# Optimization experiments

Hardware: AMD Instinct MI355X
Metric: run time of the kernel (lower is better)

Reference implementation:

```python
import jax, jax.numpy as jnp
import numpy as np

C = 768
NH = 8
S_SP = 9            # spatial size per axis; seq = 9**3 = 729
HID = (C * 4 * 2) // 3  # 2048, floor(768*8/3)
E = 3               # num_experts
TOPK = 2
EPS = 1e-5


def setup_inputs() -> dict:
    key = jax.random.key(0)
    ks = jax.random.split(key, 10)
    b = 8
    p = lambda k, shape: (jax.random.normal(k, shape, dtype=jnp.float32) * 0.02)
    return {
        "x": jax.random.normal(ks[0], (b, C, S_SP, S_SP, S_SP), dtype=jnp.float32),
        "ln_w": jnp.ones((C, S_SP, S_SP, S_SP), dtype=jnp.float32),
        "ln_b": jnp.zeros((C, S_SP, S_SP, S_SP), dtype=jnp.float32),
        "qkv_w": p(ks[1], (C, 3 * C)),
        "proj_w": p(ks[2], (C, C)),
        "router_w": p(ks[3], (C, E)),
        "gate_w": p(ks[4], (E, C, HID)),
        "up_w": p(ks[5], (E, C, HID)),
        "down_w": p(ks[6], (E, HID, C)),
    }


def _ablock(x, ln_w, ln_b, qkv_w, proj_w, router_w, gate_w, up_w, down_w):
    b, c, t, h, w = x.shape
    s = t * h * w
    dh = c // NH

    # LayerNorm over normalized_shape = (c, t, h, w)
    mean = jnp.mean(x, axis=(1, 2, 3, 4), keepdims=True)
    var = jnp.var(x, axis=(1, 2, 3, 4), keepdims=True)
    y = (x - mean) * jax.lax.rsqrt(var + EPS) * ln_w + ln_b

    # Attention (note: source applies NO 1/sqrt(dh) scaling)
    tok = jnp.transpose(y.reshape(b, c, s), (0, 2, 1))        # (b, s, c)
    qkv = (tok @ qkv_w).reshape(b, s, 3, NH, dh)
    qkv = jnp.transpose(qkv, (2, 0, 3, 1, 4))                  # (3, b, nh, s, dh)
    q, k, v = qkv[0], qkv[1], qkv[2]
    attn = jax.nn.softmax(jnp.einsum("bhsd,bhtd->bhst", q, k), axis=-1)
    o = jnp.einsum("bhst,bhtd->bhsd", attn, v)
    o = jnp.transpose(o, (0, 2, 1, 3)).reshape(b, s, c) @ proj_w  # (b, s, c)
    x = x + jnp.transpose(o, (0, 2, 1)).reshape(b, c, t, h, w)

    # MoE with top-2 routing over SwiGLU experts (dense compute)
    tok = jnp.transpose(x.reshape(b, c, s), (0, 2, 1))         # (b, s, c)
    probs = jax.nn.softmax(tok @ router_w, axis=-1)            # (b, s, E)
    vals, idx = jax.lax.top_k(probs, TOPK)
    vals = vals / jnp.sum(vals, axis=-1, keepdims=True)
    wfull = jnp.sum(jax.nn.one_hot(idx, E, dtype=tok.dtype) * vals[..., None], axis=2)  # (b, s, E)

    g = jnp.einsum("bsc,ech->bseh", tok, gate_w)
    u = jnp.einsum("bsc,ech->bseh", tok, up_w)
    hid = jax.nn.silu(g) * u                                   # (b, s, E, HID)
    eo = jnp.einsum("bseh,ehc->bsec", hid, down_w)             # (b, s, E, c)
    moe_out = jnp.einsum("bsec,bse->bsc", eo, wfull)

    return x + jnp.transpose(moe_out, (0, 2, 1)).reshape(b, c, t, h, w)


def reference(x, ln_w, ln_b, qkv_w, proj_w, router_w, gate_w, up_w, down_w):
    return _ablock(x, ln_w, ln_b, qkv_w, proj_w, router_w, gate_w, up_w, down_w)
```

## Files before the change

kernel.cpp:

```cpp
#include <hip/hip_runtime.h>
#include <hip/hip_bf16.h>

#define C_    768
#define NH_   8
#define DH_   96
#define S_    729
#define B_    8
#define MTOK  5832
#define C3    2304
#define GUN   12288
#define DK    6144
#define SPAD  736
#define NPB   559872

typedef __attribute__((ext_vector_type(8))) short short8;
typedef __attribute__((ext_vector_type(4))) float f32x4;
typedef __attribute__((ext_vector_type(4))) unsigned int uint4v;
typedef __hip_bfloat16 bf16;

__device__ __forceinline__ void gld_lds16(const bf16* g, bf16* l) {
  __builtin_amdgcn_global_load_lds((const __attribute__((address_space(1))) void*)g,
                                   (__attribute__((address_space(3))) void*)l, 16, 0, 0);
}
__device__ __forceinline__ void gld_lds16c(const char* g, char* l) {
  __builtin_amdgcn_global_load_lds((const __attribute__((address_space(1))) void*)g,
                                   (__attribute__((address_space(3))) void*)l, 16, 0, 0);
}

template<int DBO>
__device__ __forceinline__ void g97_step(
    char* ldsc, char* ldsw, const int rA, const int rB, const int cx,
    const char*& pA0, const char*& pA1, const char*& pB0, const char*& pB1,
    const bool stage, f32x4 (&acc)[4][4])
{
  const int NBO = 16384 - DBO;
  if (stage) {
    gld_lds16c(pA0, ldsw + NBO);
    gld_lds16c(pA1, ldsw + NBO + 4096);
    gld_lds16c(pB0, ldsw + NBO + 8192);
    gld_lds16c(pB1, ldsw + NBO + 12288);
    pA0 += 64; pA1 += 64; pB0 += 64; pB1 += 64;
  }
  short8 a4[4], b4[4];
  #pragma unroll
  for (int mf = 0; mf < 4; ++mf)
    a4[mf] = *(const short8*)(ldsc + DBO + rA + mf*1024 + cx);
  #pragma unroll
  for (int nf = 0; nf < 4; ++nf)
    b4[nf] = *(const short8*)(ldsc + DBO + rB + nf*1024 + cx);
  __builtin_amdgcn_s_setprio(1);
  #pragma unroll
  for (int mf = 0; mf < 4; ++mf)
    #pragma unroll
    for (int nf = 0; nf < 4; ++nf)
      acc[mf][nf] = __builtin_amdgcn_mfma_f32_16x16x32_bf16(a4[mf], b4[nf], acc[mf][nf], 0, 0, 0);
  __builtin_amdgcn_s_setprio(0);
  asm volatile("s_waitcnt vmcnt(0)" ::: "memory");
  __builtin_amdgcn_s_barrier();
}

__global__ void __launch_bounds__(256, 4)
gemm97(const bf16* __restrict__ A, long a_rs,
       const bf16* __restrict__ Bt, long b_rs,
       float* __restrict__ Cf, bf16* __restrict__ Cb,
       long c_rs, long c_zoff, int M, int N, int Ksub,
       const float* __restrict__ wfull, int mode)
{
  __shared__ __attribute__((aligned(128))) char ldsc[32768];
  const int tid = threadIdx.x;
  const int wid = tid >> 6, lid = tid & 63;
  const int wm = wid >> 1, wn = wid & 1;
  const int fr = lid & 15, g8 = (lid >> 4) * 8;
  const int brow = blockIdx.y * 128, bcol = blockIdx.x * 128;
  const long k0b = (long)blockIdx.z * Ksub * 2;
  const long a_rsb = a_rs * 2, b_rsb = b_rs * 2;
  const int srow = tid >> 2;
  const int scol = ((tid & 3) ^ ((tid >> 3) & 3)) << 4;
  const int NT = Ksub >> 5;
  char* ldsw = ldsc + wid * 1024;

  int ra0_ = brow + srow;       if (ra0_ > M-1) ra0_ = M-1;
  int ra1_ = brow + 64 + srow;  if (ra1_ > M-1) ra1_ = M-1;
  int rb0_ = bcol + srow;       if (rb0_ > N-1) rb0_ = N-1;
  int rb1_ = bcol + 64 + srow;  if (rb1_ > N-1) rb1_ = N-1;
  const char* pA0 = (const char*)A + (long)ra0_*a_rsb + k0b + scol;
  const char* pA1 = (const char*)A + (long)ra1_*a_rsb + k0b + scol;
  const char* pB0 = (const char*)Bt + (long)rb0_*b_rsb + k0b + scol;
  const char* pB1 = (const char*)Bt + (long)rb1_*b_rsb + k0b + scol;

  const int cx = (g8*2) ^ (((fr >> 1) & 3) << 4);
  const int rA = (wm*64 + fr)*64;
  const int rB = 8192 + (wn*64 + fr)*64;

  f32x4 acc[4][4] = {};

  gld_lds16c(pA0, ldsw);
  gld_lds16c(pA1, ldsw + 4096);
  gld_lds16c(pB0, ldsw + 8192);
  gld_lds16c(pB1, ldsw + 12288);
  pA0 += 64; pA1 += 64; pB0 += 64; pB1 += 64;
  asm volatile("s_waitcnt vmcnt(0)" ::: "memory");
  __builtin_amdgcn_s_barrier();

  for (int tp = 0; tp < NT; tp += 2) {
    g97_step<0>(ldsc, ldsw, rA, rB, cx, pA0, pA1, pB0, pB1, true, acc);
    g97_step<16384>(ldsc, ldsw, rA, rB, cx, pA0, pA1, pB0, pB1, (tp + 2) < NT, acc);
  }

  const int rg = (lid >> 4) * 4;
  if (mode == 3) {
    #pragma unroll
    for (int mf = 0; mf < 4; ++mf) {
      #pragma unroll
      for (int np = 0; np < 2; ++np) {
        const int hb = (bcol + wn*64 + np*32) >> 5;
        const int h = hb*16 + fr;
        const int e = h >> 11;
        #pragma unroll
        for (int j = 0; j < 4; ++j) {
          const int row = brow + wm*64 + mf*16 + rg + j;
          if (row < M) {
            float g = acc[mf][2*np][j];
            float u = acc[mf][2*np+1][j];
            float w = wfull[row*3 + e];
            float sg = g / (1.f + __expf(-g));
            Cb[(long)row*c_rs + h] = __float2bfloat16(sg * u * w);
          }
        }
      }
    }
  } else {
    #pragma unroll
    for (int mf = 0; mf < 4; ++mf) {
      #pragma unroll
      for (int nf = 0; nf < 4; ++nf) {
        const int col = bcol + wn*64 + nf*16 + fr;
        if (col < N) {
          #pragma unroll
          for (int j = 0; j < 4; ++j) {
            const int row = brow + wm*64 + mf*16 + rg + j;
            if (row < M) {
              long off = (long)blockIdx.z*c_zoff + (long)row*c_rs + col;
              if (mode == 0) Cb[off] = __float2bfloat16(acc[mf][nf][j]);
              else           Cf[off] = acc[mf][nf][j];
            }
          }
        }
      }
    }
  }
}

__global__ void __launch_bounds__(256, 3)
gemm3_bt(const bf16* __restrict__ Ah, const bf16* __restrict__ Al,
         long a_rs, long a_oo, long a_oi,
         const bf16* __restrict__ Bth, const bf16* __restrict__ Btl,
         long b_rs, long b_oo, long b_oi,
         float* __restrict__ Cf, bf16* __restrict__ Ch, bf16* __restrict__ Cl,
         long c_rs, long c_oo, long c_oi,
         int M, int N, int K, int nlim, int zdiv)
{
  __shared__ bf16 lAh[4096];
  __shared__ bf16 lAl[4096];
  __shared__ bf16 lBh[4096];
  __shared__ bf16 lBl[4096];
  const int tid = threadIdx.x;
  const int wid = tid >> 6;
  const int lid = tid & 63;
  const int z = blockIdx.z;
  const int zo = z / zdiv, zi = z - zo*zdiv;
  const long aoff = (long)zo*a_oo + (long)zi*a_oi;
  const long boff = (long)zo*b_oo + (long)zi*b_oi;
  const long cbase = (long)zo*c_oo + (long)zi*c_oi;
  const int brow = blockIdx.y * 128;
  const int bcol = blockIdx.x * 128;

  const int ch0 = tid, ch1 = tid + 256;
  int ra0 = brow + (ch0 >> 2); if (ra0 > M-1) ra0 = M-1;
  int ra1 = brow + (ch1 >> 2); if (ra1 > M-1) ra1 = M-1;
  int rb0 = bcol + (ch0 >> 2); if (rb0 > N-1) rb0 = N-1;
  int rb1 = bcol + (ch1 >> 2); if (rb1 > N-1) rb1 = N-1;
  const int sw = ((ch0 ^ (ch0 >> 3)) & 3) * 8;
  const char* qh0 = (const char*)(Ah + aoff + (long)ra0*a_rs + sw);
  const char* qh1 = (const char*)(Ah + aoff + (long)ra1*a_rs + sw);
  const char* ql0 = (const char*)(Al + aoff + (long)ra0*a_rs + sw);
  const char* ql1 = (const char*)(Al + aoff + (long)ra1*a_rs + sw);
  const char* rh0 = (const char*)(Bth + boff + (long)rb0*b_rs + sw);
  const char* rh1 = (const char*)(Bth + boff + (long)rb1*b_rs + sw);
  const char* rl0 = (const char*)(Btl + boff + (long)rb0*b_rs + sw);
  const char* rl1 = (const char*)(Btl + boff + (long)rb1*b_rs + sw);
  char* dAh0 = (char*)lAh + wid*1024;
  char* dAh1 = (char*)lAh + 4096 + wid*1024;
  char* dAl0 = (char*)lAl + wid*1024;
  char* dAl1 = (char*)lAl + 4096 + wid*1024;
  char* dBh0 = (char*)lBh + wid*1024;
  char* dBh1 = (char*)lBh + 4096 + wid*1024;
  char* dBl0 = (char*)lBl + wid*1024;
  char* dBl1 = (char*)lBl + 4096 + wid*1024;

  f32x4 acc[4][4] = {};
  const int wm = wid >> 1, wn = wid & 1;
  const int fr = lid & 15, g8 = (lid >> 4) * 8;
  const int gx = g8 ^ (((lid >> 1) & 3) << 3);

  const int NTk = K >> 5;
  for (int kt = 0; kt < NTk; ++kt) {
    __syncthreads();
    gld_lds16c(qh0, dAh0);
    gld_lds16c(qh1, dAh1);
    gld_lds16c(ql0, dAl0);
    gld_lds16c(ql1, dAl1);
    gld_lds16c(rh0, dBh0);
    gld_lds16c(rh1, dBh1);
    gld_lds16c(rl0, dBl0);
    gld_lds16c(rl1, dBl1);
    qh0 += 64; qh1 += 64; ql0 += 64; ql1 += 64;
    rh0 += 64; rh1 += 64; rl0 += 64; rl1 += 64;
    __syncthreads();
    short8 fah[4], fal[4], fbh[4], fbl[4];
    #pragma unroll
    for (int m = 0; m < 4; ++m) {
      int ro = (wm*64 + m*16 + fr)*32 + gx;
      fah[m] = *(const short8*)&lAh[ro];
      fal[m] = *(const short8*)&lAl[ro];
    }
    #pragma unroll
    for (int n = 0; n < 4; ++n) {
      int ro = (wn*64 + n*16 + fr)*32 + gx;
      fbh[n] = *(const short8*)&lBh[ro];
      fbl[n] = *(const short8*)&lBl[ro];
    }
    #pragma unroll
    for (int m = 0; m < 4; ++m)
      #pragma unroll
      for (int n = 0; n < 4; ++n) {
        acc[m][n] = __builtin_amdgcn_mfma_f32_16x16x32_bf16(fal[m], fbh[n], acc[m][n], 0, 0, 0);
        acc[m][n] = __builtin_amdgcn_mfma_f32_16x16x32_bf16(fah[m], fbl[n], acc[m][n], 0, 0, 0);
        acc[m][n] = __builtin_amdgcn_mfma_f32_16x16x32_bf16(fah[m], fbh[n], acc[m][n], 0, 0, 0);
      }
  }

  const int rg = (lid >> 4) * 4;
  #pragma unroll
  for (int m = 0; m < 4; ++m) {
    #pragma unroll
    for (int n = 0; n < 4; ++n) {
      const int col = bcol + wn*64 + n*16 + fr;
      if (col < nlim) {
        #pragma unroll
        for (int j = 0; j < 4; ++j) {
          const int row = brow + wm*64 + m*16 + rg + j;
          if (row < M) {
            long off = cbase + (long)row*c_rs + col;
            float v = acc[m][n][j];
            if (Cl) {
              bf16 h = __float2bfloat16(v);
              Ch[off] = h;
              Cl[off] = __float2bfloat16(v - __bfloat162float(h));
            } else if (Ch) {
              Ch[off] = __float2bfloat16(v);
            } else {
              Cf[off] = v;
            }
          }
        }
      }
    }
  }
}

__global__ void wtrans(const float* __restrict__ in, bf16* __restrict__ out,
                       int R, int Cc, long in_rs, long out_rs, long in_bs, long out_bs,
                       int ilv, int radd)
{
  __shared__ float tile[32][33];
  in  += (long)blockIdx.z * in_bs;
  out += (long)blockIdx.z * out_bs;
  int r0 = blockIdx.y*32, c0 = blockIdx.x*32;
  int tx = threadIdx.x, ty = threadIdx.y;
  #pragma unroll
  for (int i = 0; i < 32; i += 8) {
    int r = r0 + ty + i, c = c0 + tx;
    if (r < R && c < Cc) tile[ty+i][tx] = in[(long)r*in_rs + c];
  }
  __syncthreads();
  #pragma unroll
  for (int i = 0; i < 32; i += 8) {
    int ro = c0 + ty + i, co = r0 + tx;
    if (ro < Cc && co < R) {
      int rr = ilv ? (((ro >> 4) << 5) + (ro & 15) + radd) : ro;
      out[(long)rr*out_rs + co] = __float2bfloat16(tile[tx][ty+i]);
    }
  }
}

__global__ void wtrans3(const float* __restrict__ in, bf16* __restrict__ oh, bf16* __restrict__ ol,
                        int R, int Cc, long in_rs, long out_rs)
{
  __shared__ float tile[32][33];
  int r0 = blockIdx.y*32, c0 = blockIdx.x*32;
  int tx = threadIdx.x, ty = threadIdx.y;
  #pragma unroll
  for (int i = 0; i < 32; i += 8) {
    int r = r0 + ty + i, c = c0 + tx;
    if (r < R && c < Cc) tile[ty+i][tx] = in[(long)r*in_rs + c];
  }
  __syncthreads();
  #pragma unroll
  for (int i = 0; i < 32; i += 8) {
    int ro = c0 + ty + i, co = r0 + tx;
    if (ro < Cc && co < R) {
      float v = tile[tx][ty+i];
      bf16 h = __float2bfloat16(v);
      long o = (long)ro*out_rs + co;
      oh[o] = h;
      ol[o] = __float2bfloat16(v - __bfloat162float(h));
    }
  }
}

__global__ void ln_partial(const float* __restrict__ x, float* __restrict__ part) {
  int b = blockIdx.y, blk = blockIdx.x;
  const float* xb = x + (long)b*NPB;
  int start = blk * 4374;
  float s = 0.f, ss = 0.f;
  for (int i = start + threadIdx.x; i < start + 4374; i += 256) {
    float v = xb[i]; s += v; ss += v*v;
  }
  #pragma unroll
  for (int o = 32; o; o >>= 1) { s += __shfl_down(s, o); ss += __shfl_down(ss, o); }
  __shared__ float red[2][4];
  int wid = threadIdx.x >> 6, lid = threadIdx.x & 63;
  if (lid == 0) { red[0][wid] = s; red[1][wid] = ss; }
  __syncthreads();
  if (threadIdx.x == 0) {
    float S = 0.f, SS = 0.f;
    for (int w = 0; w < 4; ++w) { S += red[0][w]; SS += red[1][w]; }
    part[(b*128 + blk)*2] = S; part[(b*128 + blk)*2 + 1] = SS;
  }
}

__global__ void ln_final(const float* __restrict__ part, float* __restrict__ stats) {
  int b = blockIdx.x, lid = threadIdx.x;
  float s = 0.f, ss = 0.f;
  for (int i = lid; i < 128; i += 64) { s += part[(b*128+i)*2]; ss += part[(b*128+i)*2+1]; }
  #pragma unroll
  for (int o = 32; o; o >>= 1) { s += __shfl_down(s, o); ss += __shfl_down(ss, o); }
  if (lid == 0) {
    float mean = s / (float)NPB;
    float var = ss / (float)NPB - mean*mean;
    stats[b*2] = mean; stats[b*2+1] = rsqrtf(var + 1e-5f);
  }
}

__global__ void ln_apply3(const float* __restrict__ x, const float* __restrict__ lnw,
                          const float* __restrict__ lnb, const float* __restrict__ stats,
                          bf16* __restrict__ th, bf16* __restrict__ tl, long ts)
{
  __shared__ float tile[32][33];
  int b = blockIdx.z;
  int s0 = blockIdx.x*32, c0 = blockIdx.y*32;
  float mean = stats[b*2], rstd = stats[b*2+1];
  int tx = threadIdx.x, ty = threadIdx.y;
  #pragma unroll
  for (int i = 0; i < 32; i += 8) {
    int c = c0 + ty + i, s = s0 + tx;
    if (s < S_) {
      long o = (long)c*S_ + s;
      tile[ty+i][tx] = (x[(long)b*NPB + o] - mean)*rstd*lnw[o] + lnb[o];
    }
  }
  __syncthreads();
  #pragma unroll
  for (int i = 0; i < 32; i += 8) {
    int s = s0 + ty + i, c = c0 + tx;
    if (s < S_) {
      float v = tile[tx][ty+i];
      bf16 h = __float2bfloat16(v);
      long o = ((long)b*S_ + s)*ts + c;
      th[o] = h;
      tl[o] = __float2bfloat16(v - __bfloat162float(h));
    }
  }
}

__global__ void vtrans2(const bf16* __restrict__ qkvh, const bf16* __restrict__ qkvl,
                        bf16* __restrict__ VTh, bf16* __restrict__ VTl)
{
  __shared__ float tile[32][33];
  int z = blockIdx.z;
  const bf16* qkv = (z < 64) ? qkvh : qkvl;
  bf16* VT = (z < 64) ? VTh : VTl;
  int zz = z & 63;
  int bb = zz >> 3, h = zz & 7;
  const bf16* v = qkv + (long)bb*S_*C3 + 1536 + h*DH_;
  bf16* o = VT + (long)zz*DH_*SPAD;
  int t0 = blockIdx.y*32, d0 = blockIdx.x*32;
  int tx = threadIdx.x, ty = threadIdx.y;
  #pragma unroll
  for (int i = 0; i < 32; i += 8) {
    int t = t0 + ty + i, d = d0 + tx;
    float val = 0.f;
    if (t < S_ && d < DH_) val = __bfloat162float(v[(long)t*C3 + d]);
    tile[ty+i][tx] = val;
  }
  __syncthreads();
  #pragma unroll
  for (int i = 0; i < 32; i += 8) {
    int d = d0 + ty + i, t = t0 + tx;
    if (d < DH_ && t < SPAD) o[(long)d*SPAD + t] = __float2bfloat16(tile[tx][ty+i]);
  }
}

__global__ void softmax3p(bf16* __restrict__ scores, int nrows) {
  int row = blockIdx.x*4 + (threadIdx.x >> 6);
  if (row >= nrows) return;
  int lid = threadIdx.x & 63;
  bf16* ph = scores + (long)row*2*SPAD;
  bf16* pl = ph + SPAD;
  float vals[12];
  float mx = -1e30f;
  #pragma unroll
  for (int i = 0; i < 12; ++i) {
    int t = i*64 + lid;
    float v = -1e30f;
    if (t < S_) v = __bfloat162float(ph[t]) + __bfloat162float(pl[t]);
    vals[i] = v; mx = fmaxf(mx, v);
  }
  #pragma unroll
  for (int o = 32; o; o >>= 1) mx = fmaxf(mx, __shfl_xor(mx, o));
  float sum = 0.f;
  #pragma unroll
  for (int i = 0; i < 12; ++i) { float e = __expf(vals[i] - mx); vals[i] = e; sum += e; }
  #pragma unroll
  for (int o = 32; o; o >>= 1) sum += __shfl_xor(sum, o);
  float inv = 1.f / sum;
  #pragma unroll
  for (int i = 0; i < 12; ++i) {
    int t = i*64 + lid;
    if (t < SPAD) {
      float p = (t < S_) ? vals[i]*inv : 0.f;
      bf16 h = __float2bfloat16(p);
      ph[t] = h;
      pl[t] = __float2bfloat16(p - __bfloat162float(h));
    }
  }
}

__global__ void tadd1(const float* __restrict__ x, const float* __restrict__ oproj,
                      float* __restrict__ xattn, bf16* __restrict__ tok2,
                      float* __restrict__ tok2f)
{
  __shared__ float t_o[32][33];
  __shared__ float t_x[32][33];
  int b = blockIdx.z;
  int s0 = blockIdx.x*32, c0 = blockIdx.y*32;
  int tx = threadIdx.x, ty = threadIdx.y;
  #pragma unroll
  for (int i = 0; i < 32; i += 8) {
    int s = s0 + ty + i;
    if (s < S_) t_o[ty+i][tx] = oproj[((long)b*S_ + s)*C_ + c0 + tx];
    int s2 = s0 + tx;
    if (s2 < S_) t_x[ty+i][tx] = x[(long)b*NPB + (long)(c0+ty+i)*S_ + s2];
  }
  __syncthreads();
  #pragma unroll
  for (int i = 0; i < 32; i += 8) {
    int s = s0 + tx, c = c0 + ty + i;
    if (s < S_) xattn[(long)b*NPB + (long)c*S_ + s] = t_x[ty+i][tx] + t_o[tx][ty+i];
    int s2 = s0 + ty + i, c2 = c0 + tx;
    if (s2 < S_) {
      float v = t_x[tx][ty+i] + t_o[ty+i][tx];
      long o = ((long)b*S_ + s2)*C_ + c2;
      tok2[o] = __float2bfloat16(v);
      tok2f[o] = v;
    }
  }
}

__global__ void tadd2(const float* __restrict__ xattn, const bf16* __restrict__ prt,
                      float* __restrict__ out)
{
  __shared__ float t_m[32][33];
  __shared__ float t_x[32][33];
  int b = blockIdx.z;
  int s0 = blockIdx.x*32, c0 = blockIdx.y*32;
  int tx = threadIdx.x, ty = threadIdx.y;
  #pragma unroll
  for (int i = 0; i < 32; i += 8) {
    int s = s0 + ty + i;
    if (s < S_) {
      const bf16* p = prt + ((long)b*S_ + s)*768 + c0 + tx;
      float acc = 0.f;
      #pragma unroll
      for (int z = 0; z < 8; ++z) acc += __bfloat162float(p[(long)z*MTOK*768]);
      t_m[ty+i][tx] = acc;
    }
    int s2 = s0 + tx;
    if (s2 < S_) t_x[ty+i][tx] = xattn[(long)b*NPB + (long)(c0+ty+i)*S_ + s2];
  }
  __syncthreads();
  #pragma unroll
  for (int i = 0; i < 32; i += 8) {
    int s = s0 + tx, c = c0 + ty + i;
    if (s < S_) out[(long)b*NPB + (long)c*S_ + s] = t_x[ty+i][tx] + t_m[tx][ty+i];
  }
}

__global__ void router_k(const float* __restrict__ tok2f, const float* __restrict__ rw,
                         float* __restrict__ wfull)
{
  int t = blockIdx.x*4 + (threadIdx.x >> 6);
  if (t >= MTOK) return;
  int lid = threadIdx.x & 63;
  const float* tk = tok2f + (long)t*C_;
  float a0 = 0.f, a1 = 0.f, a2 = 0.f;
  for (int i = lid; i < C_; i += 64) {
    float v = tk[i];
    a0 += v*rw[i*3+0]; a1 += v*rw[i*3+1]; a2 += v*rw[i*3+2];
  }
  #pragma unroll
  for (int o = 32; o; o >>= 1) {
    a0 += __shfl_xor(a0, o); a1 += __shfl_xor(a1, o); a2 += __shfl_xor(a2, o);
  }
  if (lid == 0) {
    float m = fmaxf(a0, fmaxf(a1, a2));
    float e0 = __expf(a0-m), e1 = __expf(a1-m), e2 = __expf(a2-m);
    int emin = 0; float pm = e0;
    if (e1 <= pm) { pm = e1; emin = 1; }
    if (e2 <= pm) { pm = e2; emin = 2; }
    float rest = e0 + e1 + e2 - pm;
    wfull[t*3+0] = (emin == 0) ? 0.f : e0/rest;
    wfull[t*3+1] = (emin == 1) ? 0.f : e1/rest;
    wfull[t*3+2] = (emin == 2) ? 0.f : e2/rest;
  }
}

static inline void launch_gemm3(hipStream_t st,
    const bf16* Ah, const bf16* Al, long a_rs, long a_oo, long a_oi,
    const bf16* Bh, const bf16* Bl, long b_rs, long b_oo, long b_oi,
    float* Cf, bf16* Ch, bf16* Cl, long c_rs, long c_oo, long c_oi,
    int M, int N, int K, int nlim, int zdiv, int nz)
{
  dim3 g((N + 127)/128, (M + 127)/128, nz);
  gemm3_bt<<<g, 256, 0, st>>>(Ah, Al, a_rs, a_oo, a_oi, Bh, Bl, b_rs, b_oo, b_oi,
                              Cf, Ch, Cl, c_rs, c_oo, c_oi, M, N, K, nlim, zdiv);
}

extern "C" void kernel_launch(void* const* d_in, const int* in_sizes, int n_in,
                              void* d_out, int out_size, void* d_ws, size_t ws_size,
                              hipStream_t stream)
{
  const float* x      = (const float*)d_in[0];
  const float* ln_w   = (const float*)d_in[1];
  const float* ln_b   = (const float*)d_in[2];
  const float* qkv_w  = (const float*)d_in[3];
  const float* proj_w = (const float*)d_in[4];
  const float* rout_w = (const float*)d_in[5];
  const float* gate_w = (const float*)d_in[6];
  const float* up_w   = (const float*)d_in[7];
  const float* down_w = (const float*)d_in[8];
  float* out = (float*)d_out;

  char* ws = (char*)d_ws;
  size_t off = 0;
  auto alloc = [&](size_t bytes) { size_t r = off; off += (bytes + 255) & ~(size_t)255; return r; };

  size_t o_stats = alloc(8*2*4);
  size_t o_part  = alloc(8*128*2*4);
  size_t o_wfull = alloc((size_t)MTOK*3*4);
  size_t o_qkvTh = alloc((size_t)C3*C_*2);
  size_t o_qkvTl = alloc((size_t)C3*C_*2);
  size_t o_prjTh = alloc((size_t)C_*C_*2);
  size_t o_prjTl = alloc((size_t)C_*C_*2);
  size_t o_guT   = alloc((size_t)GUN*C_*2);
  size_t o_downT = alloc((size_t)C_*DK*2);
  size_t o_xattn = alloc((size_t)B_*NPB*4);
  size_t o_tok2  = alloc((size_t)MTOK*C_*2);
  size_t o_tok2f = alloc((size_t)MTOK*C_*4);
  size_t big0 = off;
  size_t o_qkvh  = alloc((size_t)MTOK*C3*2);
  size_t o_qkvl  = alloc((size_t)MTOK*C3*2);
  size_t o_VTh   = alloc((size_t)64*DH_*SPAD*2);
  size_t o_VTl   = alloc((size_t)64*DH_*SPAD*2);
  size_t o_aoh   = alloc((size_t)MTOK*C_*2);
  size_t o_aol   = alloc((size_t)MTOK*C_*2);
  size_t o_union = alloc((size_t)32*S_*SPAD*4);
  size_t endA = off;
  off = big0;
  size_t o_hid = alloc((size_t)MTOK*DK*2);
  size_t o_prt = alloc((size_t)8*MTOK*768*2);
  size_t endB = off;
  size_t needed = endA > endB ? endA : endB;
  if (ws_size < needed) return;

  float* stats  = (float*)(ws + o_stats);
  float* part   = (float*)(ws + o_part);
  float* wfull  = (float*)(ws + o_wfull);
  bf16*  qkvTh  = (bf16*)(ws + o_qkvTh);
  bf16*  qkvTl  = (bf16*)(ws + o_qkvTl);
  bf16*  prjTh  = (bf16*)(ws + o_prjTh);
  bf16*  prjTl  = (bf16*)(ws + o_prjTl);
  bf16*  guT    = (bf16*)(ws + o_guT);
  bf16*  downT  = (bf16*)(ws + o_downT);
  float* xattn  = (float*)(ws + o_xattn);
  bf16*  tok2   = (bf16*)(ws + o_tok2);
  float* tok2f  = (float*)(ws + o_tok2f);
  bf16*  qkvh   = (bf16*)(ws + o_qkvh);
  bf16*  qkvl   = (bf16*)(ws + o_qkvl);
  bf16*  VTh    = (bf16*)(ws + o_VTh);
  bf16*  VTl    = (bf16*)(ws + o_VTl);
  bf16*  aoh    = (bf16*)(ws + o_aoh);
  bf16*  aol    = (bf16*)(ws + o_aol);
  bf16*  tokh   = (bf16*)(ws + o_union);
  bf16*  tokl   = (bf16*)(ws + o_union + (size_t)MTOK*C_*2);
  bf16*  Pbase  = (bf16*)(ws + o_union);
  float* oproj  = (float*)(ws + o_union);
  bf16*  hidden = (bf16*)(ws + o_hid);
  bf16*  prt    = (bf16*)(ws + o_prt);

  dim3 b32(32, 8);

  wtrans3<<<dim3(72,24,1), b32, 0, stream>>>(qkv_w,  qkvTh, qkvTl, 768, 2304, 2304, 768);
  wtrans3<<<dim3(24,24,1), b32, 0, stream>>>(proj_w, prjTh, prjTl, 768, 768,  768,  768);
  wtrans<<<dim3(64,24,3), b32, 0, stream>>>(gate_w, guT, 768, 2048, 2048, 768,
                                            (long)768*2048, (long)4096*768, 1, 0);
  wtrans<<<dim3(64,24,3), b32, 0, stream>>>(up_w, guT, 768, 2048, 2048, 768,
                                            (long)768*2048, (long)4096*768, 1, 16);
  wtrans<<<dim3(24,64,3), b32, 0, stream>>>(down_w, downT, 2048, 768, 768, 6144,
                                            (long)2048*768, 2048, 0, 0);

  ln_partial<<<dim3(128,8), 256, 0, stream>>>(x, part);
  ln_final<<<8, 64, 0, stream>>>(part, stats);
  ln_apply3<<<dim3(23,24,8), b32, 0, stream>>>(x, ln_w, ln_b, stats, tokh, tokl, C_);

  launch_gemm3(stream, tokh, tokl, C_, 0, 0, qkvTh, qkvTl, C_, 0, 0,
               nullptr, qkvh, qkvl, C3, 0, 0, MTOK, C3, C_, C3, 1, 1);

  vtrans2<<<dim3(3,23,128), b32, 0, stream>>>(qkvh, qkvl, VTh, VTl);

  for (int c = 0; c < 2; ++c) {
    const long qoff = (long)(4*c)*S_*C3;
    launch_gemm3(stream,
        qkvh + qoff, qkvl + qoff, C3, (long)S_*C3, DH_,
        qkvh + qoff + 768, qkvl + qoff + 768, C3, (long)S_*C3, DH_,
        nullptr, Pbase, Pbase + SPAD, 2*SPAD, (long)8*S_*2*SPAD, (long)S_*2*SPAD,
        S_, S_, DH_, SPAD, 8, 32);
    softmax3p<<<5832, 256, 0, stream>>>(Pbase, 32*S_);
    launch_gemm3(stream,
        Pbase, Pbase + SPAD, 2*SPAD, (long)8*S_*2*SPAD, (long)S_*2*SPAD,
        VTh + (size_t)c*32*DH_*SPAD, VTl + (size_t)c*32*DH_*SPAD, SPAD,
        (long)8*DH_*SPAD, (long)DH_*SPAD,
        nullptr, aoh + (size_t)(4*c)*S_*C_, aol + (size_t)(4*c)*S_*C_,
        C_, (long)S_*C_, DH_,
        S_, DH_, SPAD, DH_, 8, 32);
  }

  launch_gemm3(stream, aoh, aol, C_, 0, 0, prjTh, prjTl, C_, 0, 0,
               oproj, nullptr, nullptr, C_, 0, 0, MTOK, C_, C_, C_, 1, 1);

  tadd1<<<dim3(23,24,8), b32, 0, stream>>>(x, oproj, xattn, tok2, tok2f);

  router_k<<<1458, 256, 0, stream>>>(tok2f, rout_w, wfull);

  gemm97<<<dim3(GUN/128, 46, 1), 256, 0, stream>>>(
      tok2, C_, guT, C_, nullptr, hidden, DK, 0, MTOK, GUN, C_, wfull, 3);

  gemm97<<<dim3(C_/128, 46, 8), 256, 0, stream>>>(
      hidden, DK, downT, DK, nullptr, prt, 768, (long)MTOK*768, MTOK, C_, DK/8,
      nullptr, 0);

  tadd2<<<dim3(23,24,8), b32, 0, stream>>>(xattn, prt, out);
}
```

Before: 727.3 us.

## Double-buffer LDS in split-bf16 gemm3 kernel to overlap loads with MFMA

Rewrites the three-pass split-bf16 GEMM main loop to use two 32 KB LDS buffers. The next K-tile is issued via global_load_lds while MFMAs run on the current one, and there is one barrier per step instead of two. It also raises MFMA wave priority during compute. The larger LDS footprint lowers the occupancy bound from 3 to 2 blocks per CU, and the swizzle and row mapping change.

```diff
diff --git a/kernel.cpp b/kernel.cpp
--- a/kernel.cpp
+++ b/kernel.cpp
@@ -18,10 +18,6 @@
 typedef __attribute__((ext_vector_type(4))) unsigned int uint4v;
 typedef __hip_bfloat16 bf16;
 
-__device__ __forceinline__ void gld_lds16(const bf16* g, bf16* l) {
-  __builtin_amdgcn_global_load_lds((const __attribute__((address_space(1))) void*)g,
-                                   (__attribute__((address_space(3))) void*)l, 16, 0, 0);
-}
 __device__ __forceinline__ void gld_lds16c(const char* g, char* l) {
   __builtin_amdgcn_global_load_lds((const __attribute__((address_space(1))) void*)g,
                                    (__attribute__((address_space(3))) void*)l, 16, 0, 0);
@@ -151,7 +147,54 @@
   }
 }
 
-__global__ void __launch_bounds__(256, 3)
+template<int DBO>
+__device__ __forceinline__ void g3_step(
+    char* ldsc, char* ldsw, const int wm, const int wn, const int cx, const int fr,
+    const char*& qh0, const char*& qh1, const char*& ql0, const char*& ql1,
+    const char*& rh0, const char*& rh1, const char*& rl0, const char*& rl1,
+    const bool stage, f32x4 (&acc)[4][4])
+{
+  const int NBO = 32768 - DBO;
+  if (stage) {
+    gld_lds16c(qh0, ldsw + NBO);
+    gld_lds16c(qh1, ldsw + NBO + 4096);
+    gld_lds16c(ql0, ldsw + NBO + 8192);
+    gld_lds16c(ql1, ldsw + NBO + 12288);
+    gld_lds16c(rh0, ldsw + NBO + 16384);
+    gld_lds16c(rh1, ldsw + NBO + 20480);
+    gld_lds16c(rl0, ldsw + NBO + 24576);
+    gld_lds16c(rl1, ldsw + NBO + 28672);
+    qh0 += 64; qh1 += 64; ql0 += 64; ql1 += 64;
+    rh0 += 64; rh1 += 64; rl0 += 64; rl1 += 64;
+  }
+  short8 fah[4], fal[4], fbh[4], fbl[4];
+  #pragma unroll
+  for (int m = 0; m < 4; ++m) {
+    const int ro = DBO + (wm*64 + m*16 + fr)*64 + cx;
+    fah[m] = *(const short8*)(ldsc + ro);
+    fal[m] = *(const short8*)(ldsc + ro + 8192);
+  }
+  #pragma unroll
+  for (int n = 0; n < 4; ++n) {
+    const int ro = DBO + 16384 + (wn*64 + n*16 + fr)*64 + cx;
+    fbh[n] = *(const short8*)(ldsc + ro);
+    fbl[n] = *(const short8*)(ldsc + ro + 8192);
+  }
+  __builtin_amdgcn_s_setprio(1);
+  #pragma unroll
+  for (int m = 0; m < 4; ++m)
+    #pragma unroll
+    for (int n = 0; n < 4; ++n) {
+      acc[m][n] = __builtin_amdgcn_mfma_f32_16x16x32_bf16(fal[m], fbh[n], acc[m][n], 0, 0, 0);
+      acc[m][n] = __builtin_amdgcn_mfma_f32_16x16x32_bf16(fah[m], fbl[n], acc[m][n], 0, 0, 0);
+      acc[m][n] = __builtin_amdgcn_mfma_f32_16x16x32_bf16(fah[m], fbh[n], acc[m][n], 0, 0, 0);
+    }
+  __builtin_amdgcn_s_setprio(0);
+  asm volatile("s_waitcnt vmcnt(0)" ::: "memory");
+  __builtin_amdgcn_s_barrier();
+}
+
+__global__ void __launch_bounds__(256, 2)
 gemm3_bt(const bf16* __restrict__ Ah, const bf16* __restrict__ Al,
          long a_rs, long a_oo, long a_oi,
          const bf16* __restrict__ Bth, const bf16* __restrict__ Btl,
@@ -160,10 +203,7 @@
          long c_rs, long c_oo, long c_oi,
          int M, int N, int K, int nlim, int zdiv)
 {
-  __shared__ bf16 lAh[4096];
-  __shared__ bf16 lAl[4096];
-  __shared__ bf16 lBh[4096];
-  __shared__ bf16 lBl[4096];
+  __shared__ __attribute__((aligned(128))) char ldsc[65536];
   const int tid = threadIdx.x;
   const int wid = tid >> 6;
   const int lid = tid & 63;
@@ -175,11 +215,11 @@
   const int brow = blockIdx.y * 128;
   const int bcol = blockIdx.x * 128;
 
-  const int ch0 = tid, ch1 = tid + 256;
-  int ra0 = brow + (ch0 >> 2); if (ra0 > M-1) ra0 = M-1;
-  int ra1 = brow + (ch1 >> 2); if (ra1 > M-1) ra1 = M-1;
-  int rb0 = bcol + (ch0 >> 2); if (rb0 > N-1) rb0 = N-1;
-  int rb1 = bcol + (ch1 >> 2); if (rb1 > N-1) rb1 = N-1;
+  const int ch0 = tid;
+  int ra0 = brow + (ch0 >> 2);       if (ra0 > M-1) ra0 = M-1;
+  int ra1 = brow + 64 + (ch0 >> 2);  if (ra1 > M-1) ra1 = M-1;
+  int rb0 = bcol + (ch0 >> 2);       if (rb0 > N-1) rb0 = N-1;
+  int rb1 = bcol + 64 + (ch0 >> 2);  if (rb1 > N-1) rb1 = N-1;
   const int sw = ((ch0 ^ (ch0 >> 3)) & 3) * 8;
   const char* qh0 = (const char*)(Ah + aoff + (long)ra0*a_rs + sw);
   const char* qh1 = (const char*)(Ah + aoff + (long)ra1*a_rs + sw);
@@ -189,55 +229,33 @@
   const char* rh1 = (const char*)(Bth + boff + (long)rb1*b_rs + sw);
   const char* rl0 = (const char*)(Btl + boff + (long)rb0*b_rs + sw);
   const char* rl1 = (const char*)(Btl + boff + (long)rb1*b_rs + sw);
-  char* dAh0 = (char*)lAh + wid*1024;
-  char* dAh1 = (char*)lAh + 4096 + wid*1024;
-  char* dAl0 = (char*)lAl + wid*1024;
-  char* dAl1 = (char*)lAl + 4096 + wid*1024;
-  char* dBh0 = (char*)lBh + wid*1024;
-  char* dBh1 = (char*)lBh + 4096 + wid*1024;
-  char* dBl0 = (char*)lBl + wid*1024;
-  char* dBl1 = (char*)lBl + 4096 + wid*1024;
+  char* ldsw = ldsc + wid * 1024;
 
   f32x4 acc[4][4] = {};
   const int wm = wid >> 1, wn = wid & 1;
   const int fr = lid & 15, g8 = (lid >> 4) * 8;
-  const int gx = g8 ^ (((lid >> 1) & 3) << 3);
-
-  const int NTk = K >> 5;
-  for (int kt = 0; kt < NTk; ++kt) {
-    __syncthreads();
-    gld_lds16c(qh0, dAh0);
-    gld_lds16c(qh1, dAh1);
-    gld_lds16c(ql0, dAl0);
-    gld_lds16c(ql1, dAl1);
-    gld_lds16c(rh0, dBh0);
-    gld_lds16c(rh1, dBh1);
-    gld_lds16c(rl0, dBl0);
-    gld_lds16c(rl1, dBl1);
-    qh0 += 64; qh1 += 64; ql0 += 64; ql1 += 64;
-    rh0 += 64; rh1 += 64; rl0 += 64; rl1 += 64;
-    __syncthreads();
-    short8 fah[4], fal[4], fbh[4], fbl[4];
-    #pragma unroll
-    for (int m = 0; m < 4; ++m) {
-      int ro = (wm*64 + m*16 + fr)*32 + gx;
-      fah[m] = *(const short8*)&lAh[ro];
-      fal[m] = *(const short8*)&lAl[ro];
-    }
-    #pragma unroll
-    for (int n = 0; n < 4; ++n) {
-      int ro = (wn*64 + n*16 + fr)*32 + gx;
-      fbh[n] = *(const short8*)&lBh[ro];
-      fbl[n] = *(const short8*)&lBl[ro];
-    }
-    #pragma unroll
-    for (int m = 0; m < 4; ++m)
-      #pragma unroll
-      for (int n = 0; n < 4; ++n) {
-        acc[m][n] = __builtin_amdgcn_mfma_f32_16x16x32_bf16(fal[m], fbh[n], acc[m][n], 0, 0, 0);
-        acc[m][n] = __builtin_amdgcn_mfma_f32_16x16x32_bf16(fah[m], fbl[n], acc[m][n], 0, 0, 0);
-        acc[m][n] = __builtin_amdgcn_mfma_f32_16x16x32_bf16(fah[m], fbh[n], acc[m][n], 0, 0, 0);
-      }
+  const int cx = (g8*2) ^ (((fr >> 1) & 3) << 4);
+
+  const int NT = K >> 5;
+  gld_lds16c(qh0, ldsw);
+  gld_lds16c(qh1, ldsw + 4096);
+  gld_lds16c(ql0, ldsw + 8192);
+  gld_lds16c(ql1, ldsw + 12288);
+  gld_lds16c(rh0, ldsw + 16384);
+  gld_lds16c(rh1, ldsw + 20480);
+  gld_lds16c(rl0, ldsw + 24576);
+  gld_lds16c(rl1, ldsw + 28672);
+  qh0 += 64; qh1 += 64; ql0 += 64; ql1 += 64;
+  rh0 += 64; rh1 += 64; rl0 += 64; rl1 += 64;
+  asm volatile("s_waitcnt vmcnt(0)" ::: "memory");
+  __builtin_amdgcn_s_barrier();
+
+  for (int tp = 0; tp < NT; tp += 2) {
+    g3_step<0>(ldsc, ldsw, wm, wn, cx, fr,
+               qh0, qh1, ql0, ql1, rh0, rh1, rl0, rl1, (tp + 1) < NT, acc);
+    if (tp + 1 < NT)
+      g3_step<32768>(ldsc, ldsw, wm, wn, cx, fr,
+                     qh0, qh1, ql0, ql1, rh0, rh1, rl0, rl1, (tp + 2) < NT, acc);
   }
 
   const int rg = (lid >> 4) * 4;
```

New measurement: 701.0 us. 3.6% less time.
